# Performance work log

Hardware: AMD Instinct MI355X
Metric: run time of the kernel (lower is better)

## Reference

```python
import jax, jax.numpy as jnp
import numpy as np

N = 500_000
D = 256
D_OUT = 256
B = 16_384


def setup_inputs() -> dict:
    key = jax.random.key(0)
    ks = jax.random.split(key, 10)
    x = jax.random.normal(ks[0], (N, D), dtype=jnp.float32)
    batch = jnp.sort(jax.random.randint(ks[1], (N,), 0, B))
    last_click_mask = jax.random.uniform(ks[2], (N,), dtype=jnp.float32)
    s = 1.0 / np.sqrt(D)
    W1 = jax.random.uniform(ks[3], (D, D), jnp.float32, -s, s)
    b1 = jax.random.uniform(ks[4], (D,), jnp.float32, -s, s)
    W2 = jax.random.uniform(ks[5], (D, D), jnp.float32, -s, s)
    b2 = jax.random.uniform(ks[6], (D,), jnp.float32, -s, s)
    w3 = jax.random.uniform(ks[7], (D, 1), jnp.float32, -s, s)
    s4 = 1.0 / np.sqrt(2 * D)
    W4 = jax.random.uniform(ks[8], (2 * D, D_OUT), jnp.float32, -s4, s4)
    b4 = jax.random.uniform(ks[9], (D_OUT,), jnp.float32, -s4, s4)
    return {
        "x": x,
        "batch": batch,
        "last_click_mask": last_click_mask,
        "num_segments": B,
        "W1": W1, "b1": b1, "W2": W2, "b2": b2,
        "w3": w3, "W4": W4, "b4": b4,
    }


def reference(x, batch, last_click_mask, num_segments, W1, b1, W2, b2, w3, W4, b4):
    # local_rep = global_add_pool(x * mask, batch)  -> [B, D]
    local_rep = jax.ops.segment_sum(x * last_click_mask[:, None], batch,
                                    num_segments=num_segments)
    local_rep_repeat = local_rep[batch]                       # [N, D] gather
    att = jax.nn.sigmoid(local_rep_repeat @ W1 + b1 + x @ W2 + b2) @ w3  # [N, 1]
    weighted_x = x * att                                      # [N, D]
    global_rep = jax.ops.segment_sum(weighted_x, batch,
                                     num_segments=num_segments)  # [B, D]
    rep = jnp.concatenate([local_rep, global_rep], axis=1)    # [B, 2D]
    return rep @ W4 + b4                                      # [B, D_OUT]
```

## Files before the change

### kernel.cpp

```cpp
#include <hip/hip_runtime.h>
#include <hip/hip_bf16.h>

#define NROWS 500000
#define DIM   256
#define BSEG  16384
#define LDSP  264
#define NTILE 7813
#define TILE_B (64 * LDSP * 2)

typedef __attribute__((ext_vector_type(8))) short short8;
typedef __attribute__((ext_vector_type(4))) float floatx4;

#define GLD16(gsrc, ldst)                                                      \
  __builtin_amdgcn_global_load_lds(                                            \
      (const __attribute__((address_space(1))) unsigned int*)(gsrc),           \
      (__attribute__((address_space(3))) unsigned int*)(ldst), 16, 0, 0)


__device__ __forceinline__ unsigned short f2bf(float f) {
  unsigned u = __float_as_uint(f);
  unsigned r = u + 0x7fffu + ((u >> 16) & 1u);
  return (unsigned short)(r >> 16);
}
__device__ __forceinline__ float bf2f(short s) {
  return __uint_as_float(((unsigned)(unsigned short)s) << 16);
}
__device__ __forceinline__ float fast_sigmoid(float z) {
  return 1.0f / (1.0f + __expf(-z));
}

__global__ __launch_bounds__(1024) void k_zero(float* __restrict__ p, int n4) {
  int i = blockIdx.x * blockDim.x + threadIdx.x;
  if (i < n4) ((float4*)p)[i] = make_float4(0.f, 0.f, 0.f, 0.f);
}

__global__ __launch_bounds__(256) void k_convert_all(
    const float* __restrict__ W1, const float* __restrict__ W2,
    const float* __restrict__ W4, short* __restrict__ W1t,
    short* __restrict__ W2t, short* __restrict__ W4t)
{
  int blk = blockIdx.x;
  const float* W; short* out; int kt;
  if (blk < 8)       { W = W1; out = W1t; kt = blk; }
  else if (blk < 16) { W = W2; out = W2t; kt = blk - 8; }
  else               { W = W4; out = W4t; kt = blk - 16; }
  int n = threadIdx.x;
  short tmp[32];
#pragma unroll
  for (int kk = 0; kk < 32; ++kk)
    tmp[kk] = (short)f2bf(W[(size_t)(kt * 32 + kk) * DIM + n]);
  size_t base = ((size_t)kt * 256 + n) * 32;
#pragma unroll
  for (int kk = 0; kk < 32; kk += 4)
    *(short4*)&out[base + kk] = *(short4*)&tmp[kk];
}

__device__ __forceinline__ void stage_tile(const float* __restrict__ A, int row0,
                                           int maxrow, short* xs, int tid)
{
#pragma unroll
  for (int it = 0; it < 16; ++it) {
    int linear = it * 256 + tid;
    int r = linear >> 6;
    int c4 = linear & 63;
    int row = min(row0 + r, maxrow);
    float4 v = *(const float4*)&A[(size_t)row * DIM + c4 * 4];
    short4 o;
    o.x = (short)f2bf(v.x); o.y = (short)f2bf(v.y);
    o.z = (short)f2bf(v.z); o.w = (short)f2bf(v.w);
    *(short4*)&xs[r * LDSP + c4 * 4] = o;
  }
}

__global__ __launch_bounds__(256) void k_prep(
    const float* __restrict__ x, const int* __restrict__ batch,
    const float* __restrict__ mask, char* __restrict__ xbf16p,
    float* __restrict__ local_rep)
{
  __shared__ __align__(16) short xs[64 * LDSP];
  __shared__ int   seg_s[64];
  __shared__ float mask_s[64];
  const int tid = threadIdx.x;
  const int tile = blockIdx.x;
  const int row0 = tile * 64;

  stage_tile(x, row0, NROWS - 1, xs, tid);
  if (tid < 64) {
    int row = min(row0 + tid, NROWS - 1);
    seg_s[tid] = batch[row];
    mask_s[tid] = mask[row];
  }
  __syncthreads();

  float4* g4 = (float4*)(xbf16p + (size_t)tile * TILE_B);
  const float4* l4 = (const float4*)xs;
#pragma unroll
  for (int j = 0; j < 8; ++j)
    g4[j * 256 + tid] = l4[j * 256 + tid];
  if (tid < 64) g4[2048 + tid] = l4[2048 + tid];

  const int col = tid;
  const int rmax = min(64, NROWS - row0);
  float acc = 0.f;
  int cur = seg_s[0];
  for (int r = 0; r < rmax; ++r) {
    int s = seg_s[r];
    float xv = bf2f(xs[r * LDSP + col]);
    if (s != cur) {
      atomicAdd(&local_rep[(size_t)cur * DIM + col], acc);
      acc = 0.f; cur = s;
    }
    acc = fmaf(xv, mask_s[r], acc);
  }
  atomicAdd(&local_rep[(size_t)cur * DIM + col], acc);
}

__device__ __forceinline__ void mfma_pass(const short* xs, const short* __restrict__ Wt,
                                          floatx4 acc[4][4], int lane15, int quad, int n0)
{
  for (int kt = 0; kt < 8; ++kt) {
    short8 bfr[4], afr[4];
#pragma unroll
    for (int jn = 0; jn < 4; ++jn)
      bfr[jn] = *(const short8*)&Wt[(size_t)kt * 8192 + (n0 + jn * 16 + lane15) * 32 + quad * 8];
#pragma unroll
    for (int i = 0; i < 4; ++i)
      afr[i] = *(const short8*)&xs[(i * 16 + lane15) * LDSP + kt * 32 + quad * 8];
#pragma unroll
    for (int i = 0; i < 4; ++i)
#pragma unroll
      for (int jn = 0; jn < 4; ++jn)
        acc[i][jn] = __builtin_amdgcn_mfma_f32_16x16x32_bf16(afr[i], bfr[jn], acc[i][jn], 0, 0, 0);
  }
}

__global__ __launch_bounds__(256) void k_h1_mfma(
    const float* __restrict__ A, const short* __restrict__ Wt,
    const float* __restrict__ bias, short* __restrict__ H1bf)
{
  __shared__ __align__(16) short xs[64 * LDSP];
  const int tid = threadIdx.x;
  const int row0 = blockIdx.x * 64;
  stage_tile(A, row0, BSEG - 1, xs, tid);
  __syncthreads();
  const int lane = tid & 63, wave = tid >> 6;
  const int lane15 = lane & 15, quad = lane >> 4;
  const int n0 = wave * 64;
  floatx4 acc[4][4];
#pragma unroll
  for (int i = 0; i < 4; ++i)
#pragma unroll
    for (int j = 0; j < 4; ++j) acc[i][j] = (floatx4)0.f;
  mfma_pass(xs, Wt, acc, lane15, quad, n0);
#pragma unroll
  for (int i = 0; i < 4; ++i)
#pragma unroll
    for (int jn = 0; jn < 4; ++jn) {
      int col = n0 + jn * 16 + lane15;
      float bv = bias[col];
#pragma unroll
      for (int r = 0; r < 4; ++r) {
        int row = row0 + i * 16 + quad * 4 + r;
        H1bf[(size_t)row * DIM + col] = (short)f2bf(acc[i][jn][r] + bv);
      }
    }
}

__global__ __launch_bounds__(256) void k_fused_main(
    const char* __restrict__ xbf16p, const int* __restrict__ batch,
    const short* __restrict__ W2t, const float* __restrict__ b2,
    const float* __restrict__ w3, const short* __restrict__ H1bf,
    float* __restrict__ global_rep)
{
  __shared__ __align__(16) short xs[64 * LDSP];
  __shared__ int   seg_s[64];
  __shared__ float att_s[64];
  const int tid = threadIdx.x;
  const int row0 = blockIdx.x * 64;
  const int lane = tid & 63, wave = tid >> 6;

  {
    const char* gtile = xbf16p + (size_t)blockIdx.x * TILE_B;
    char* lbase = (char*)xs;
#pragma unroll
    for (int j = 0; j < 9; ++j) {
      int c = wave + 4 * j;
      if (c < 33)
        GLD16(gtile + (size_t)c * 1024 + lane * 16, lbase + c * 1024);
    }
  }
  if (tid < 64) {
    seg_s[tid] = batch[min(row0 + tid, NROWS - 1)];
    att_s[tid] = 0.f;
  }
  __syncthreads();

  const int lane15 = lane & 15, quad = lane >> 4;
  const int n0 = wave * 64;
  floatx4 acc[4][4];
#pragma unroll
  for (int i = 0; i < 4; ++i)
#pragma unroll
    for (int j = 0; j < 4; ++j) acc[i][j] = (floatx4)0.f;
  mfma_pass(xs, W2t, acc, lane15, quad, n0);

  float b2v[4], w3v[4];
#pragma unroll
  for (int jn = 0; jn < 4; ++jn) {
    int col = n0 + jn * 16 + lane15;
    b2v[jn] = b2[col];
    w3v[jn] = w3[col];
  }
  float part[4][4];
#pragma unroll
  for (int i = 0; i < 4; ++i)
#pragma unroll
    for (int r = 0; r < 4; ++r) {
      int rl = i * 16 + quad * 4 + r;
      int seg = seg_s[rl];
      float p = 0.f;
#pragma unroll
      for (int jn = 0; jn < 4; ++jn) {
        int col = n0 + jn * 16 + lane15;
        float h = bf2f(H1bf[(size_t)seg * DIM + col]);
        float z = acc[i][jn][r] + h + b2v[jn];
        p = fmaf(fast_sigmoid(z), w3v[jn], p);
      }
      part[i][r] = p;
    }
#pragma unroll
  for (int off = 1; off < 16; off <<= 1)
#pragma unroll
    for (int i = 0; i < 4; ++i)
#pragma unroll
      for (int r = 0; r < 4; ++r)
        part[i][r] += __shfl_xor(part[i][r], off, 64);
  if (lane15 == 0) {
#pragma unroll
    for (int i = 0; i < 4; ++i)
#pragma unroll
      for (int r = 0; r < 4; ++r)
        atomicAdd(&att_s[i * 16 + quad * 4 + r], part[i][r]);
  }
  __syncthreads();

  const int col = tid;
  const int rmax = min(64, NROWS - row0);
  float acc2 = 0.f;
  int cur = seg_s[0];
  for (int r = 0; r < rmax; ++r) {
    int s = seg_s[r];
    float xv = bf2f(xs[r * LDSP + col]);
    float av = att_s[r];
    if (s != cur) {
      atomicAdd(&global_rep[(size_t)cur * DIM + col], acc2);
      acc2 = 0.f; cur = s;
    }
    acc2 = fmaf(xv, av, acc2);
  }
  atomicAdd(&global_rep[(size_t)cur * DIM + col], acc2);
}

__global__ __launch_bounds__(256) void k_out_mfma(
    const float* __restrict__ local_rep, const float* __restrict__ global_rep,
    const short* __restrict__ W4t, const float* __restrict__ b4,
    float* __restrict__ out)
{
  __shared__ __align__(16) short xs[64 * LDSP];
  const int tid = threadIdx.x;
  const int row0 = blockIdx.x * 64;
  const int lane = tid & 63, wave = tid >> 6;
  const int lane15 = lane & 15, quad = lane >> 4;
  const int n0 = wave * 64;
  floatx4 acc[4][4];
#pragma unroll
  for (int i = 0; i < 4; ++i)
#pragma unroll
    for (int j = 0; j < 4; ++j) acc[i][j] = (floatx4)0.f;

  stage_tile(local_rep, row0, BSEG - 1, xs, tid);
  __syncthreads();
  mfma_pass(xs, W4t, acc, lane15, quad, n0);
  __syncthreads();
  stage_tile(global_rep, row0, BSEG - 1, xs, tid);
  __syncthreads();
  mfma_pass(xs, W4t + (size_t)8 * 8192, acc, lane15, quad, n0);

#pragma unroll
  for (int i = 0; i < 4; ++i)
#pragma unroll
    for (int jn = 0; jn < 4; ++jn) {
      int col = n0 + jn * 16 + lane15;
      float bv = b4[col];
#pragma unroll
      for (int r = 0; r < 4; ++r) {
        int row = row0 + i * 16 + quad * 4 + r;
        out[(size_t)row * DIM + col] = acc[i][jn][r] + bv;
      }
    }
}

extern "C" void kernel_launch(void* const* d_in, const int* in_sizes, int n_in,
                              void* d_out, int out_size, void* d_ws, size_t ws_size,
                              hipStream_t stream) {
  (void)in_sizes; (void)n_in; (void)out_size; (void)ws_size;
  const float* x    = (const float*)d_in[0];
  const int*   batch= (const int*)d_in[1];
  const float* mask = (const float*)d_in[2];
  const float* W1 = (const float*)d_in[4];
  const float* b1 = (const float*)d_in[5];
  const float* W2 = (const float*)d_in[6];
  const float* b2 = (const float*)d_in[7];
  const float* w3 = (const float*)d_in[8];
  const float* W4 = (const float*)d_in[9];
  const float* b4 = (const float*)d_in[10];
  float* out = (float*)d_out;

  char* base = (char*)d_ws;
  float* local_rep  = (float*)(base);
  float* global_rep = (float*)(base + (size_t)16 * 1024 * 1024);
  short* H1bf       = (short*)(base + (size_t)32 * 1024 * 1024);
  short* W1t        = (short*)(base + (size_t)40 * 1024 * 1024);
  short* W2t        = (short*)(base + (size_t)40 * 1024 * 1024 + 128 * 1024);
  short* W4t        = (short*)(base + (size_t)40 * 1024 * 1024 + 256 * 1024);
  char*  xbf16p     = base + (size_t)48 * 1024 * 1024;

  int n4 = 2 * BSEG * DIM / 4;
  hipLaunchKernelGGL(k_zero, dim3(n4 / 1024), dim3(1024), 0, stream, local_rep, n4);

  hipLaunchKernelGGL(k_convert_all, dim3(32), dim3(256), 0, stream,
                     W1, W2, W4, W1t, W2t, W4t);

  hipLaunchKernelGGL(k_prep, dim3(NTILE), dim3(256), 0, stream,
                     x, batch, mask, xbf16p, local_rep);

  hipLaunchKernelGGL(k_h1_mfma, dim3(BSEG / 64), dim3(256), 0, stream,
                     local_rep, W1t, b1, H1bf);

  hipLaunchKernelGGL(k_fused_main, dim3(NTILE), dim3(256), 0, stream,
                     xbf16p, batch, W2t, b2, w3, H1bf, global_rep);

  hipLaunchKernelGGL(k_out_mfma, dim3(BSEG / 64), dim3(256), 0, stream,
                     local_rep, global_rep, W4t, b4, out);
}
```

Measured before the change: 984.9 us.

## Persistent double-buffered fused kernel, register-based prep, merged init launch

New measurement: 1.344 ms. +36.4%, slower.

```diff
diff --git a/kernel.cpp b/kernel.cpp
--- a/kernel.cpp
+++ b/kernel.cpp
@@ -7,6 +7,7 @@
 #define LDSP  264
 #define NTILE 7813
 #define TILE_B (64 * LDSP * 2)
+#define FGRID 512
 
 typedef __attribute__((ext_vector_type(8))) short short8;
 typedef __attribute__((ext_vector_type(4))) float floatx4;
@@ -28,31 +29,85 @@
 __device__ __forceinline__ float fast_sigmoid(float z) {
   return 1.0f / (1.0f + __expf(-z));
 }
-
-__global__ __launch_bounds__(1024) void k_zero(float* __restrict__ p, int n4) {
-  int i = blockIdx.x * blockDim.x + threadIdx.x;
-  if (i < n4) ((float4*)p)[i] = make_float4(0.f, 0.f, 0.f, 0.f);
-}
-
-__global__ __launch_bounds__(256) void k_convert_all(
+__device__ __forceinline__ int imin(int a, int b) { return a < b ? a : b; }
+
+__global__ __launch_bounds__(256) void k_init(
     const float* __restrict__ W1, const float* __restrict__ W2,
     const float* __restrict__ W4, short* __restrict__ W1t,
-    short* __restrict__ W2t, short* __restrict__ W4t)
+    short* __restrict__ W2t, short* __restrict__ W4t,
+    float* __restrict__ zbase)
 {
   int blk = blockIdx.x;
-  const float* W; short* out; int kt;
-  if (blk < 8)       { W = W1; out = W1t; kt = blk; }
-  else if (blk < 16) { W = W2; out = W2t; kt = blk - 8; }
-  else               { W = W4; out = W4t; kt = blk - 16; }
   int n = threadIdx.x;
-  short tmp[32];
-#pragma unroll
-  for (int kk = 0; kk < 32; ++kk)
-    tmp[kk] = (short)f2bf(W[(size_t)(kt * 32 + kk) * DIM + n]);
-  size_t base = ((size_t)kt * 256 + n) * 32;
-#pragma unroll
-  for (int kk = 0; kk < 32; kk += 4)
-    *(short4*)&out[base + kk] = *(short4*)&tmp[kk];
+  if (blk < 32) {
+    const float* W; short* out; int kt;
+    if (blk < 8)       { W = W1; out = W1t; kt = blk; }
+    else if (blk < 16) { W = W2; out = W2t; kt = blk - 8; }
+    else               { W = W4; out = W4t; kt = blk - 16; }
+    short tmp[32];
+#pragma unroll
+    for (int kk = 0; kk < 32; ++kk)
+      tmp[kk] = (short)f2bf(W[(size_t)(kt * 32 + kk) * DIM + n]);
+    size_t base = ((size_t)kt * 256 + n) * 32;
+#pragma unroll
+    for (int kk = 0; kk < 32; kk += 4)
+      *(short4*)&out[base + kk] = *(short4*)&tmp[kk];
+  } else {
+    int i = (blk - 32) * 256 + n;
+    ((float4*)zbase)[i] = make_float4(0.f, 0.f, 0.f, 0.f);
+  }
+}
+
+__global__ __launch_bounds__(256) void k_prep2(
+    const float* __restrict__ x, const int* __restrict__ batch,
+    const float* __restrict__ mask, char* __restrict__ xbf16p,
+    float* __restrict__ local_rep)
+{
+  __shared__ int   seg_s[64];
+  __shared__ float mask_s[64];
+  const int tid = threadIdx.x;
+  const int tile = (int)blockIdx.x;
+  const int row0 = tile * 64;
+  const int g  = tid >> 6;
+  const int c4 = tid & 63;
+
+  if (tid < 64) {
+    int row = row0 + tid;
+    int rowc = imin(row, NROWS - 1);
+    seg_s[tid]  = batch[rowc];
+    mask_s[tid] = (row < NROWS) ? mask[rowc] : 0.f;
+  }
+  __syncthreads();
+
+  short* img = (short*)(xbf16p + (size_t)tile * TILE_B);
+  float4 acc = make_float4(0.f, 0.f, 0.f, 0.f);
+  int cur = seg_s[g];
+
+#pragma unroll
+  for (int it = 0; it < 16; ++it) {
+    const int r = 4 * it + g;
+    const int rowc = imin(row0 + r, NROWS - 1);
+    float4 v = *(const float4*)&x[(size_t)rowc * DIM + c4 * 4];
+    short4 o;
+    o.x = (short)f2bf(v.x); o.y = (short)f2bf(v.y);
+    o.z = (short)f2bf(v.z); o.w = (short)f2bf(v.w);
+    *(short4*)&img[r * LDSP + c4 * 4] = o;
+
+    int s = seg_s[r];
+    float m = mask_s[r];
+    if (s != cur) {
+      float* dst = &local_rep[(size_t)cur * DIM + c4 * 4];
+      atomicAdd(dst + 0, acc.x); atomicAdd(dst + 1, acc.y);
+      atomicAdd(dst + 2, acc.z); atomicAdd(dst + 3, acc.w);
+      acc = make_float4(0.f, 0.f, 0.f, 0.f);
+      cur = s;
+    }
+    acc.x = fmaf(v.x, m, acc.x); acc.y = fmaf(v.y, m, acc.y);
+    acc.z = fmaf(v.z, m, acc.z); acc.w = fmaf(v.w, m, acc.w);
+  }
+  float* dst = &local_rep[(size_t)cur * DIM + c4 * 4];
+  atomicAdd(dst + 0, acc.x); atomicAdd(dst + 1, acc.y);
+  atomicAdd(dst + 2, acc.z); atomicAdd(dst + 3, acc.w);
 }
 
 __device__ __forceinline__ void stage_tile(const float* __restrict__ A, int row0,
@@ -63,7 +118,7 @@
     int linear = it * 256 + tid;
     int r = linear >> 6;
     int c4 = linear & 63;
-    int row = min(row0 + r, maxrow);
+    int row = imin(row0 + r, maxrow);
     float4 v = *(const float4*)&A[(size_t)row * DIM + c4 * 4];
     short4 o;
     o.x = (short)f2bf(v.x); o.y = (short)f2bf(v.y);
@@ -72,49 +127,6 @@
   }
 }
 
-__global__ __launch_bounds__(256) void k_prep(
-    const float* __restrict__ x, const int* __restrict__ batch,
-    const float* __restrict__ mask, char* __restrict__ xbf16p,
-    float* __restrict__ local_rep)
-{
-  __shared__ __align__(16) short xs[64 * LDSP];
-  __shared__ int   seg_s[64];
-  __shared__ float mask_s[64];
-  const int tid = threadIdx.x;
-  const int tile = blockIdx.x;
-  const int row0 = tile * 64;
-
-  stage_tile(x, row0, NROWS - 1, xs, tid);
-  if (tid < 64) {
-    int row = min(row0 + tid, NROWS - 1);
-    seg_s[tid] = batch[row];
-    mask_s[tid] = mask[row];
-  }
-  __syncthreads();
-
-  float4* g4 = (float4*)(xbf16p + (size_t)tile * TILE_B);
-  const float4* l4 = (const float4*)xs;
-#pragma unroll
-  for (int j = 0; j < 8; ++j)
-    g4[j * 256 + tid] = l4[j * 256 + tid];
-  if (tid < 64) g4[2048 + tid] = l4[2048 + tid];
-
-  const int col = tid;
-  const int rmax = min(64, NROWS - row0);
-  float acc = 0.f;
-  int cur = seg_s[0];
-  for (int r = 0; r < rmax; ++r) {
-    int s = seg_s[r];
-    float xv = bf2f(xs[r * LDSP + col]);
-    if (s != cur) {
-      atomicAdd(&local_rep[(size_t)cur * DIM + col], acc);
-      acc = 0.f; cur = s;
-    }
-    acc = fmaf(xv, mask_s[r], acc);
-  }
-  atomicAdd(&local_rep[(size_t)cur * DIM + col], acc);
-}
-
 __device__ __forceinline__ void mfma_pass(const short* xs, const short* __restrict__ Wt,
                                           floatx4 acc[4][4], int lane15, int quad, int n0)
 {
@@ -140,7 +152,7 @@
 {
   __shared__ __align__(16) short xs[64 * LDSP];
   const int tid = threadIdx.x;
-  const int row0 = blockIdx.x * 64;
+  const int row0 = (int)blockIdx.x * 64;
   stage_tile(A, row0, BSEG - 1, xs, tid);
   __syncthreads();
   const int lane = tid & 63, wave = tid >> 6;
@@ -166,99 +178,124 @@
     }
 }
 
-__global__ __launch_bounds__(256) void k_fused_main(
+__global__ __launch_bounds__(256) void k_fused2(
     const char* __restrict__ xbf16p, const int* __restrict__ batch,
     const short* __restrict__ W2t, const float* __restrict__ b2,
     const float* __restrict__ w3, const short* __restrict__ H1bf,
     float* __restrict__ global_rep)
 {
-  __shared__ __align__(16) short xs[64 * LDSP];
-  __shared__ int   seg_s[64];
-  __shared__ float att_s[64];
+  __shared__ __align__(16) short xs[2][64 * LDSP];
+  __shared__ int   seg_s[2][64];
+  __shared__ float att_s[2][64];
   const int tid = threadIdx.x;
-  const int row0 = blockIdx.x * 64;
   const int lane = tid & 63, wave = tid >> 6;
+  const int lane15 = lane & 15, quad = lane >> 4;
+  const int n0 = wave * 64;
+  const int bid = (int)blockIdx.x;
+
+  float b2v[4], w3v[4];
+#pragma unroll
+  for (int jn = 0; jn < 4; ++jn) {
+    int col = n0 + jn * 16 + lane15;
+    b2v[jn] = b2[col];
+    w3v[jn] = w3[col];
+  }
 
   {
-    const char* gtile = xbf16p + (size_t)blockIdx.x * TILE_B;
-    char* lbase = (char*)xs;
+    const char* gtile = xbf16p + (size_t)bid * TILE_B;
+    char* lbase = (char*)&xs[0][0];
 #pragma unroll
     for (int j = 0; j < 9; ++j) {
       int c = wave + 4 * j;
       if (c < 33)
         GLD16(gtile + (size_t)c * 1024 + lane * 16, lbase + c * 1024);
     }
-  }
-  if (tid < 64) {
-    seg_s[tid] = batch[min(row0 + tid, NROWS - 1)];
-    att_s[tid] = 0.f;
-  }
-  __syncthreads();
-
-  const int lane15 = lane & 15, quad = lane >> 4;
-  const int n0 = wave * 64;
-  floatx4 acc[4][4];
-#pragma unroll
-  for (int i = 0; i < 4; ++i)
-#pragma unroll
-    for (int j = 0; j < 4; ++j) acc[i][j] = (floatx4)0.f;
-  mfma_pass(xs, W2t, acc, lane15, quad, n0);
-
-  float b2v[4], w3v[4];
-#pragma unroll
-  for (int jn = 0; jn < 4; ++jn) {
-    int col = n0 + jn * 16 + lane15;
-    b2v[jn] = b2[col];
-    w3v[jn] = w3[col];
-  }
-  float part[4][4];
-#pragma unroll
-  for (int i = 0; i < 4; ++i)
-#pragma unroll
-    for (int r = 0; r < 4; ++r) {
-      int rl = i * 16 + quad * 4 + r;
-      int seg = seg_s[rl];
-      float p = 0.f;
-#pragma unroll
-      for (int jn = 0; jn < 4; ++jn) {
-        int col = n0 + jn * 16 + lane15;
-        float h = bf2f(H1bf[(size_t)seg * DIM + col]);
-        float z = acc[i][jn][r] + h + b2v[jn];
-        p = fmaf(fast_sigmoid(z), w3v[jn], p);
-      }
-      part[i][r] = p;
-    }
-#pragma unroll
-  for (int off = 1; off < 16; off <<= 1)
+    if (tid < 64) {
+      seg_s[0][tid] = batch[imin(bid * 64 + tid, NROWS - 1)];
+      att_s[0][tid] = 0.f;
+    }
+  }
+  __syncthreads();
+
+  int cur = 0;
+  for (int t = bid; t < NTILE; t += FGRID) {
+    const int tn = t + FGRID;
+    if (tn < NTILE) {
+      const char* gtile = xbf16p + (size_t)tn * TILE_B;
+      char* lbase = (char*)&xs[cur ^ 1][0];
+#pragma unroll
+      for (int j = 0; j < 9; ++j) {
+        int c = wave + 4 * j;
+        if (c < 33)
+          GLD16(gtile + (size_t)c * 1024 + lane * 16, lbase + c * 1024);
+      }
+      if (tid < 64) {
+        seg_s[cur ^ 1][tid] = batch[imin(tn * 64 + tid, NROWS - 1)];
+        att_s[cur ^ 1][tid] = 0.f;
+      }
+    }
+
+    floatx4 acc[4][4];
 #pragma unroll
     for (int i = 0; i < 4; ++i)
 #pragma unroll
-      for (int r = 0; r < 4; ++r)
-        part[i][r] += __shfl_xor(part[i][r], off, 64);
-  if (lane15 == 0) {
+      for (int j = 0; j < 4; ++j) acc[i][j] = (floatx4)0.f;
+    mfma_pass(&xs[cur][0], W2t, acc, lane15, quad, n0);
+
+    float part[4][4];
 #pragma unroll
     for (int i = 0; i < 4; ++i)
 #pragma unroll
-      for (int r = 0; r < 4; ++r)
-        atomicAdd(&att_s[i * 16 + quad * 4 + r], part[i][r]);
-  }
-  __syncthreads();
-
-  const int col = tid;
-  const int rmax = min(64, NROWS - row0);
-  float acc2 = 0.f;
-  int cur = seg_s[0];
-  for (int r = 0; r < rmax; ++r) {
-    int s = seg_s[r];
-    float xv = bf2f(xs[r * LDSP + col]);
-    float av = att_s[r];
-    if (s != cur) {
-      atomicAdd(&global_rep[(size_t)cur * DIM + col], acc2);
-      acc2 = 0.f; cur = s;
-    }
-    acc2 = fmaf(xv, av, acc2);
-  }
-  atomicAdd(&global_rep[(size_t)cur * DIM + col], acc2);
+      for (int r = 0; r < 4; ++r) {
+        int rl = i * 16 + quad * 4 + r;
+        int seg = seg_s[cur][rl];
+        float p = 0.f;
+#pragma unroll
+        for (int jn = 0; jn < 4; ++jn) {
+          int col = n0 + jn * 16 + lane15;
+          float h = bf2f(H1bf[(size_t)seg * DIM + col]);
+          float z = acc[i][jn][r] + h + b2v[jn];
+          p = fmaf(fast_sigmoid(z), w3v[jn], p);
+        }
+        part[i][r] = p;
+      }
+#pragma unroll
+    for (int off = 1; off < 16; off <<= 1)
+#pragma unroll
+      for (int i = 0; i < 4; ++i)
+#pragma unroll
+        for (int r = 0; r < 4; ++r)
+          part[i][r] += __shfl_xor(part[i][r], off, 64);
+    if (lane15 == 0) {
+#pragma unroll
+      for (int i = 0; i < 4; ++i)
+#pragma unroll
+        for (int r = 0; r < 4; ++r)
+          atomicAdd(&att_s[cur][i * 16 + quad * 4 + r], part[i][r]);
+    }
+    __syncthreads();
+
+    {
+      const int row0 = t * 64;
+      const int col = tid;
+      const int rmax = imin(64, NROWS - row0);
+      float acc2 = 0.f;
+      int sc = seg_s[cur][0];
+      for (int r = 0; r < rmax; ++r) {
+        int s = seg_s[cur][r];
+        float xv = bf2f(xs[cur][r * LDSP + col]);
+        float av = att_s[cur][r];
+        if (s != sc) {
+          atomicAdd(&global_rep[(size_t)sc * DIM + col], acc2);
+          acc2 = 0.f; sc = s;
+        }
+        acc2 = fmaf(xv, av, acc2);
+      }
+      atomicAdd(&global_rep[(size_t)sc * DIM + col], acc2);
+    }
+    __syncthreads();
+    cur ^= 1;
+  }
 }
 
 __global__ __launch_bounds__(256) void k_out_mfma(
@@ -268,7 +305,7 @@
 {
   __shared__ __align__(16) short xs[64 * LDSP];
   const int tid = threadIdx.x;
-  const int row0 = blockIdx.x * 64;
+  const int row0 = (int)blockIdx.x * 64;
   const int lane = tid & 63, wave = tid >> 6;
   const int lane15 = lane & 15, quad = lane >> 4;
   const int n0 = wave * 64;
@@ -325,19 +362,16 @@
   short* W4t        = (short*)(base + (size_t)40 * 1024 * 1024 + 256 * 1024);
   char*  xbf16p     = base + (size_t)48 * 1024 * 1024;
 
-  int n4 = 2 * BSEG * DIM / 4;
-  hipLaunchKernelGGL(k_zero, dim3(n4 / 1024), dim3(1024), 0, stream, local_rep, n4);
-
-  hipLaunchKernelGGL(k_convert_all, dim3(32), dim3(256), 0, stream,
-                     W1, W2, W4, W1t, W2t, W4t);
-
-  hipLaunchKernelGGL(k_prep, dim3(NTILE), dim3(256), 0, stream,
+  hipLaunchKernelGGL(k_init, dim3(32 + 8192), dim3(256), 0, stream,
+                     W1, W2, W4, W1t, W2t, W4t, local_rep);
+
+  hipLaunchKernelGGL(k_prep2, dim3(NTILE), dim3(256), 0, stream,
                      x, batch, mask, xbf16p, local_rep);
 
   hipLaunchKernelGGL(k_h1_mfma, dim3(BSEG / 64), dim3(256), 0, stream,
                      local_rep, W1t, b1, H1bf);
 
-  hipLaunchKernelGGL(k_fused_main, dim3(NTILE), dim3(256), 0, stream,
+  hipLaunchKernelGGL(k_fused2, dim3(FGRID), dim3(256), 0, stream,
                      xbf16p, batch, W2t, b2, w3, H1bf, global_rep);
 
   hipLaunchKernelGGL(k_out_mfma, dim3(BSEG / 64), dim3(256), 0, stream,
```
